# Kernel tuning notes

Hardware: AMD Instinct MI355X
Metric: run time of the kernel (lower is better)

The kernel has to match this reference:

```python
import jax, jax.numpy as jnp
import numpy as np

N_NODES = 100000
N_EDGES = 250000
D = 384
N_ETYPES = 8


def setup_inputs() -> dict:
    key = jax.random.key(0)
    k_h, k_u, k_v, k_e, k_w = jax.random.split(key, 5)
    h = jax.random.normal(k_h, (N_NODES, D), dtype=jnp.float32)
    u = jax.random.randint(k_u, (N_EDGES,), 0, N_NODES, dtype=jnp.int64)
    v = jax.random.randint(k_v, (N_EDGES,), 0, N_NODES, dtype=jnp.int64)
    etype = jax.random.randint(k_e, (N_EDGES,), 0, N_ETYPES, dtype=jnp.int64)
    # xavier_normal_ with relu gain: std = gain * sqrt(2 / (fan_in + fan_out))
    gain = float(np.sqrt(2.0))
    std = gain * np.sqrt(2.0 / (N_ETYPES + D))
    rel_weight = jax.random.normal(k_w, (N_ETYPES, D), dtype=jnp.float32) * std
    return {"h": h, "u": u, "v": v, "etype": etype, "rel_weight": rel_weight}


def reference(h, u, v, etype, rel_weight):
    # Per-edge DistMult score: sigmoid(sum_d h[u,d] * R[etype,d] * h[v,d])
    emb_u = h[u]                     # [E, D] gather
    emb_v = h[v]                     # [E, D] gather
    rel = rel_weight[etype]          # [E, D] gather
    score = jnp.sum(emb_u * rel * emb_v, axis=1)  # [E]
    return jax.nn.sigmoid(score)
```

## Files before the change

### kernel.cpp

```cpp
#include <hip/hip_runtime.h>
#include <math.h>


#define D 384
#define LANES_PER_EDGE 16

__global__ __launch_bounds__(256) void distmult_kernel(
    const float* __restrict__ h,
    const int* __restrict__ u,
    const int* __restrict__ v,
    const int* __restrict__ etype,
    const float* __restrict__ rel,
    float* __restrict__ out,
    int n_edges)
{
    int tid  = blockIdx.x * blockDim.x + threadIdx.x;
    int e    = tid >> 4;
    int lane = threadIdx.x & 15;
    if (e >= n_edges) return;

    const float4* hu = (const float4*)(h   + (size_t)u[e]     * D);
    const float4* hv = (const float4*)(h   + (size_t)v[e]     * D);
    const float4* r  = (const float4*)(rel + (size_t)etype[e] * D);

    float4 a[6], b[6], c[6];
#pragma unroll
    for (int k = 0; k < 6; ++k) {
        int j = lane + k * 16;
        a[k] = hu[j];
        b[k] = hv[j];
        c[k] = r[j];
    }

    float s = 0.0f;
#pragma unroll
    for (int k = 0; k < 6; ++k) {
        s += a[k].x * c[k].x * b[k].x;
        s += a[k].y * c[k].y * b[k].y;
        s += a[k].z * c[k].z * b[k].z;
        s += a[k].w * c[k].w * b[k].w;
    }

#pragma unroll
    for (int off = 8; off >= 1; off >>= 1)
        s += __shfl_xor(s, off);

    if (lane == 0)
        out[e] = 1.0f / (1.0f + __expf(-s));
}

extern "C" void kernel_launch(void* const* d_in, const int* in_sizes, int n_in,
                              void* d_out, int out_size, void* d_ws, size_t ws_size,
                              hipStream_t stream) {
    const float* h     = (const float*)d_in[0];
    const int*   u     = (const int*)  d_in[1];
    const int*   v     = (const int*)  d_in[2];
    const int*   etype = (const int*)  d_in[3];
    const float* rel   = (const float*)d_in[4];
    float* out = (float*)d_out;

    int n_edges = in_sizes[1];
    long long threads_total = (long long)n_edges * LANES_PER_EDGE;
    int block = 256;
    int grid = (int)((threads_total + block - 1) / block);
    distmult_kernel<<<grid, block, 0, stream>>>(h, u, v, etype, rel, out, n_edges);
}
```

Baseline: 281.7 us.

## Convert node embeddings and relation weights to bf16 before gather-dot

Adds a pre-pass that converts the full h table and the relation weights to bf16 in workspace, then has the edge kernel gather half-width rows and unpack them to fp32 for the triple product. The aim is to halve the bytes moved by the random row gathers. In exchange it reads all of h and writes a bf16 copy every call, which is about as much traffic as the gathers themselves. It also lowers precision of the inputs.

```diff
diff --git a/kernel.cpp b/kernel.cpp
--- a/kernel.cpp
+++ b/kernel.cpp
@@ -1,16 +1,38 @@
 #include <hip/hip_runtime.h>
+#include <hip/hip_bf16.h>
 #include <math.h>
 
 
 #define D 384
-#define LANES_PER_EDGE 16
+#define N_NODES_ELEMS (100000 * 384)
+#define H_BF16_BYTES  (100000 * 384 * 2)
+
+__global__ __launch_bounds__(256) void conv_h_kernel(
+    const float* __restrict__ src, uint32_t* __restrict__ dst, int n8)
+{
+    int i = blockIdx.x * blockDim.x + threadIdx.x;
+    if (i >= n8) return;
+    const float4* s = (const float4*)(src) + (size_t)i * 2;
+    float4 f0 = s[0];
+    float4 f1 = s[1];
+    uint4 o;
+    o.x = (uint32_t)__bfloat16_as_ushort(__float2bfloat16(f0.x)) |
+          ((uint32_t)__bfloat16_as_ushort(__float2bfloat16(f0.y)) << 16);
+    o.y = (uint32_t)__bfloat16_as_ushort(__float2bfloat16(f0.z)) |
+          ((uint32_t)__bfloat16_as_ushort(__float2bfloat16(f0.w)) << 16);
+    o.z = (uint32_t)__bfloat16_as_ushort(__float2bfloat16(f1.x)) |
+          ((uint32_t)__bfloat16_as_ushort(__float2bfloat16(f1.y)) << 16);
+    o.w = (uint32_t)__bfloat16_as_ushort(__float2bfloat16(f1.z)) |
+          ((uint32_t)__bfloat16_as_ushort(__float2bfloat16(f1.w)) << 16);
+    ((uint4*)dst)[i] = o;
+}
 
 __global__ __launch_bounds__(256) void distmult_kernel(
-    const float* __restrict__ h,
+    const uint32_t* __restrict__ hb,
+    const uint32_t* __restrict__ rb,
     const int* __restrict__ u,
     const int* __restrict__ v,
     const int* __restrict__ etype,
-    const float* __restrict__ rel,
     float* __restrict__ out,
     int n_edges)
 {
@@ -19,13 +41,13 @@
     int lane = threadIdx.x & 15;
     if (e >= n_edges) return;
 
-    const float4* hu = (const float4*)(h   + (size_t)u[e]     * D);
-    const float4* hv = (const float4*)(h   + (size_t)v[e]     * D);
-    const float4* r  = (const float4*)(rel + (size_t)etype[e] * D);
+    const uint4* hu = (const uint4*)(hb + (size_t)u[e]     * (D / 2));
+    const uint4* hv = (const uint4*)(hb + (size_t)v[e]     * (D / 2));
+    const uint4* r  = (const uint4*)(rb + (size_t)etype[e] * (D / 2));
 
-    float4 a[6], b[6], c[6];
+    uint4 a[3], b[3], c[3];
 #pragma unroll
-    for (int k = 0; k < 6; ++k) {
+    for (int k = 0; k < 3; ++k) {
         int j = lane + k * 16;
         a[k] = hu[j];
         b[k] = hv[j];
@@ -34,11 +56,21 @@
 
     float s = 0.0f;
 #pragma unroll
-    for (int k = 0; k < 6; ++k) {
-        s += a[k].x * c[k].x * b[k].x;
-        s += a[k].y * c[k].y * b[k].y;
-        s += a[k].z * c[k].z * b[k].z;
-        s += a[k].w * c[k].w * b[k].w;
+    for (int k = 0; k < 3; ++k) {
+        const uint32_t* pa = &a[k].x;
+        const uint32_t* pb = &b[k].x;
+        const uint32_t* pc = &c[k].x;
+#pragma unroll
+        for (int q = 0; q < 4; ++q) {
+            float alo = __uint_as_float(pa[q] << 16);
+            float ahi = __uint_as_float(pa[q] & 0xffff0000u);
+            float blo = __uint_as_float(pb[q] << 16);
+            float bhi = __uint_as_float(pb[q] & 0xffff0000u);
+            float clo = __uint_as_float(pc[q] << 16);
+            float chi = __uint_as_float(pc[q] & 0xffff0000u);
+            s += alo * clo * blo;
+            s += ahi * chi * bhi;
+        }
     }
 
 #pragma unroll
@@ -60,8 +92,17 @@
     float* out = (float*)d_out;
 
     int n_edges = in_sizes[1];
-    long long threads_total = (long long)n_edges * LANES_PER_EDGE;
-    int block = 256;
-    int grid = (int)((threads_total + block - 1) / block);
-    distmult_kernel<<<grid, block, 0, stream>>>(h, u, v, etype, rel, out, n_edges);
+    int n_rel   = in_sizes[4];
+
+    uint32_t* hb = (uint32_t*)d_ws;
+    uint32_t* rb = (uint32_t*)((char*)d_ws + H_BF16_BYTES);
+
+    int n8_h = N_NODES_ELEMS / 8;
+    conv_h_kernel<<<(n8_h + 255) / 256, 256, 0, stream>>>(h, hb, n8_h);
+    int n8_r = n_rel / 8;
+    conv_h_kernel<<<(n8_r + 255) / 256, 256, 0, stream>>>(rel, rb, n8_r);
+
+    long long threads_total = (long long)n_edges * 16;
+    int grid = (int)((threads_total + 255) / 256);
+    distmult_kernel<<<grid, 256, 0, stream>>>(hb, rb, u, v, etype, out, n_edges);
 }
```

Result: no change. 278.8 us (-1.0%).
